# Optimization experiments

Measured on AMD Instinct MI355X. Metric: run time of the kernel, lower is better.

Reference implementation:

```python
import jax, jax.numpy as jnp
import numpy as np

EPS = 1e-13

def masked_softmax(x, mask):
    # Non-memory-efficient path of the original: softmax(x*mask), re-mask, renormalize.
    p = jax.nn.softmax(x * mask, axis=-1) * mask
    return p / (jnp.sum(p, axis=-1, keepdims=True) + EPS)

def setup_inputs() -> dict:
    key = jax.random.key(0)
    ka, kb, kma, kmb = jax.random.split(key, 4)
    B, La, Lb, D = 32, 1024, 1024, 256
    a = jax.random.normal(ka, (B, La, D), dtype=jnp.float32)
    b = jax.random.normal(kb, (B, Lb, D), dtype=jnp.float32)
    mask_a = jax.random.randint(kma, (B, La, 1), 0, 2, dtype=jnp.int32)
    mask_b = jax.random.randint(kmb, (B, Lb, 1), 0, 2, dtype=jnp.int32)
    return {"a": a, "b": b, "mask_a": mask_a, "mask_b": mask_b}

def reference(a, b, mask_a, mask_b):
    # a: [B, La, D], b: [B, Lb, D], mask_a: [B, La, 1], mask_b: [B, Lb, 1]
    ma = mask_a.astype(a.dtype)  # [B, La, 1]
    mb = mask_b.astype(b.dtype)  # [B, Lb, 1]
    attn = jnp.einsum('bid,bjd->bij', a, b)            # [B, La, Lb]
    amask = ma * jnp.swapaxes(mb, 1, 2)                 # outer product mask [B, La, Lb]
    weight_for_a = masked_softmax(attn, amask)          # softmax over Lb
    attended_a = jnp.einsum('bij,bjd->bid', weight_for_a, b)  # [B, La, D]
    attn_t = jnp.swapaxes(attn, 1, 2)                   # [B, Lb, La]
    amask_t = jnp.swapaxes(amask, 1, 2)
    weight_for_b = masked_softmax(attn_t, amask_t)      # softmax over La
    attended_b = jnp.einsum('bji,bid->bjd', weight_for_b, a)  # [B, Lb, D]
    return (attended_a, attended_b)
```

## Files before the change

### kernel.cpp

```cpp
#include <hip/hip_runtime.h>
#include <math.h>
#include <stdint.h>


#define NB    32
#define SEQ   1024
#define DIM   256
#define BM    128
#define BN    64
#define SHIFT 60.0f
#define PS    1048

typedef unsigned int uint;
typedef unsigned short ushort;
typedef __attribute__((ext_vector_type(8)))  short short8;
typedef __attribute__((ext_vector_type(16))) float f32x16;

#define HL_BATCH  (64 * 1024 * 8)
#define HL_TENSOR ((size_t)NB * HL_BATCH)
#define T_BATCH   (128 * 256 * 8)
#define T_TENSOR  ((size_t)NB * T_BATCH)
#define WS_NEED   ((2 * HL_TENSOR + 2 * T_TENSOR) * sizeof(ushort))

__device__ __forceinline__ ushort bf16_rn(float x) {
    union { float f; uint u; } v; v.f = x;
    uint r = v.u + 0x7fffu + ((v.u >> 16) & 1u);
    return (ushort)(r >> 16);
}
__device__ __forceinline__ float bf16_to_f(ushort h) {
    union { uint u; float f; } v; v.u = ((uint)h) << 16;
    return v.f;
}
__device__ __forceinline__ void gl_lds16(const ushort* g, ushort* l) {
    __builtin_amdgcn_global_load_lds(
        (const __attribute__((address_space(1))) void*)g,
        (__attribute__((address_space(3))) void*)l, 16, 0, 0);
}

#define TSTR 264
__global__ __launch_bounds__(256)
void prepass(const float* __restrict__ A, const float* __restrict__ Bt,
             ushort* __restrict__ aHL, ushort* __restrict__ bHL,
             ushort* __restrict__ aT,  ushort* __restrict__ bT)
{
    const int tensor = blockIdx.z;
    const float* src = tensor ? Bt : A;
    ushort* hl = tensor ? bHL : aHL;
    ushort* tp = tensor ? bT  : aT;
    const int batch = blockIdx.y;
    const int tid   = threadIdx.x;

    __shared__ float tile[8 * TSTR];

    ushort* hlb = hl + (size_t)batch * HL_BATCH;

    for (int it = 0; it < 8; ++it) {
        const int soct = blockIdx.x * 8 + it;
        const int s0   = soct * 8;
        if (it) __syncthreads();

        {
            const int oct = tid >> 3, srow = tid & 7;
            const float* rp = src + ((size_t)batch * SEQ + s0 + srow) * DIM + oct * 8;
            float4 x0 = *(const float4*)rp;
            float4 x1 = *(const float4*)(rp + 4);
            float xs[8] = {x0.x, x0.y, x0.z, x0.w, x1.x, x1.y, x1.z, x1.w};
            short8 hv, lv;
            #pragma unroll
            for (int j = 0; j < 8; ++j) {
                ushort h = bf16_rn(xs[j]);
                hv[j] = (short)h;
                lv[j] = (short)bf16_rn(xs[j] - bf16_to_f(h));
            }
            *(short8*)(hlb + (size_t)oct * 8192 + (size_t)(s0 + srow) * 8)        = hv;
            *(short8*)(hlb + (size_t)(oct + 32) * 8192 + (size_t)(s0 + srow) * 8) = lv;
        }

        const float* sb = src + ((size_t)batch * SEQ + s0) * DIM;
        #pragma unroll
        for (int i = 0; i < 2; ++i) {
            int idx = tid + i * 256;
            int r = idx >> 6, c = idx & 63;
            float4 v = *((const float4*)(sb + (size_t)r * DIM) + c);
            *(float4*)&tile[r * TSTR + c * 4] = v;
        }
        __syncthreads();
        {
            ushort* tpb = tp + (size_t)batch * T_BATCH + (size_t)soct * 2048;
            int d = tid;
            short8 hv;
            #pragma unroll
            for (int j = 0; j < 8; ++j)
                hv[j] = (short)bf16_rn(tile[j * TSTR + d]);
            *(short8*)(tpb + (size_t)d * 8) = hv;
        }
    }
}

__global__ __launch_bounds__(512, 2)
void attend3(const ushort* __restrict__ aHL, const ushort* __restrict__ bHL,
             const ushort* __restrict__ aT,  const ushort* __restrict__ bT,
             const int*    __restrict__ ma,  const int*    __restrict__ mb,
             float*        __restrict__ out)
{
    __shared__ __align__(16) ushort Ks2[64 * 512];
    __shared__ __align__(16) ushort Vt2[8 * 2048];
    __shared__ __align__(16) ushort Ph[8 * PS];
    __shared__ float msk[SEQ];
    __shared__ float lpart[2][BM];
    __shared__ float invs[BM];

    const int bx   = blockIdx.x;
    const int xcd  = bx & 7;
    const int slot = bx >> 3;
    const int rb   = slot & 7;
    const int pg   = slot >> 3;
    const int pair = xcd + 8 * pg;
    const int batch = pair >> 1;
    const int dir   = pair & 1;
    const int row0  = rb * BM;

    const ushort* hlX = dir ? bHL : aHL;
    const ushort* hlY = dir ? aHL : bHL;
    const ushort* tY  = dir ? aT  : bT;
    const int*    mx  = dir ? mb  : ma;
    const int*    my  = dir ? ma  : mb;
    float* o = out + (size_t)dir * NB * SEQ * DIM;

    const int tid  = threadIdx.x;
    const int lane = tid & 63;
    const int wave = tid >> 6;
    const int l31  = lane & 31;
    const int lh   = lane >> 5;
    const int rw   = wave >> 1;
    const int cw   = wave & 1;

    const ushort* hlXb = hlX + (size_t)batch * HL_BATCH;
    const ushort* hlYb = hlY + (size_t)batch * HL_BATCH;
    const ushort* tYb  = tY  + (size_t)batch * T_BATCH;

    const ushort* ksrc = hlYb + (size_t)(wave * 8) * 8192 + (size_t)lane * 8;
    ushort*       kdst = Ks2 + wave * 8 * 512 + lane * 8;
    const ushort* vsrc = tYb + (size_t)wave * 2048 + (size_t)lane * 8;
    ushort*       vdst = Vt2 + wave * 2048 + lane * 8;

    #pragma unroll
    for (int i = 0; i < 8; ++i) gl_lds16(ksrc + (size_t)i * 8192, kdst + i * 512);
    #pragma unroll
    for (int i = 0; i < 4; ++i) gl_lds16(vsrc + i * 512, vdst + i * 512);

    for (int i = tid; i < SEQ; i += 512) msk[i] = (float)my[batch * SEQ + i];

    const int qrow = row0 + rw * 32 + l31;
    short8 qhi[16], qlo[16];
    {
        const ushort* qb = hlXb + (size_t)lh * 8192 + (size_t)qrow * 8;
        #pragma unroll
        for (int kk = 0; kk < 16; ++kk) {
            qhi[kk] = *(const short8*)(qb + (size_t)(2 * kk) * 8192);
            qlo[kk] = *(const short8*)(qb + (size_t)(2 * kk + 32) * 8192);
        }
    }

    f32x16 oacc[4];
    #pragma unroll
    for (int t = 0; t < 4; ++t)
        #pragma unroll
        for (int r = 0; r < 16; ++r) oacc[t][r] = 0.f;
    float lsum[16];
    #pragma unroll
    for (int r = 0; r < 16; ++r) lsum[r] = 0.f;

    __syncthreads();

    for (int nt = 0; nt < SEQ / BN; ++nt) {
        const int key0 = nt * BN;
        const float mkv = msk[key0 + cw * 32 + l31];

        f32x16 a1, a2;
        #pragma unroll
        for (int r = 0; r < 16; ++r) { a1[r] = 0.f; a2[r] = 0.f; }
        const int kcol = (cw * 32 + l31) * 8;
        #pragma unroll
        for (int kk = 0; kk < 16; ++kk) {
            short8 bhi = *(const short8*)&Ks2[(2 * kk + lh) * 512 + kcol];
            a1 = __builtin_amdgcn_mfma_f32_32x32x16_bf16(qhi[kk], bhi, a1, 0, 0, 0);
            a2 = __builtin_amdgcn_mfma_f32_32x32x16_bf16(qlo[kk], bhi, a2, 0, 0, 0);
        }
        #pragma unroll
        for (int kk = 0; kk < 16; ++kk) {
            short8 blo = *(const short8*)&Ks2[(2 * kk + lh + 32) * 512 + kcol];
            a2 = __builtin_amdgcn_mfma_f32_32x32x16_bf16(qhi[kk], blo, a2, 0, 0, 0);
        }

        const int key  = cw * 32 + l31;
        const int koct = key >> 3, kj = key & 7;
        #pragma unroll
        for (int r = 0; r < 16; ++r) {
            float s = a1[r] + a2[r];
            float p = __expf(s - SHIFT) * mkv;
            lsum[r] += p;
            int qr = rw * 32 + (r & 3) + ((r >> 2) << 3) + (lh << 2);
            Ph[koct * PS + qr * 8 + kj] = bf16_rn(p);
        }
        __syncthreads();

        if (nt + 1 < SEQ / BN) {
            const ushort* ks = ksrc + (size_t)(key0 + BN) * 8;
            #pragma unroll
            for (int i = 0; i < 8; ++i) gl_lds16(ks + (size_t)i * 8192, kdst + i * 512);
        }

        const int prow = (rw * 32 + l31) * 8;
        #pragma unroll
        for (int kb = 0; kb < 4; ++kb) {
            short8 pa = *(const short8*)&Ph[(2 * kb + lh) * PS + prow];
            #pragma unroll
            for (int t = 0; t < 4; ++t) {
                int dim = cw * 128 + t * 32 + l31;
                short8 vf = *(const short8*)&Vt2[(2 * kb + lh) * 2048 + dim * 8];
                oacc[t] = __builtin_amdgcn_mfma_f32_32x32x16_bf16(pa, vf, oacc[t], 0, 0, 0);
            }
        }
        __syncthreads();

        if (nt + 1 < SEQ / BN) {
            const ushort* vs = vsrc + ((size_t)(key0 + BN) >> 3) * 2048;
            #pragma unroll
            for (int i = 0; i < 4; ++i) gl_lds16(vs + i * 512, vdst + i * 512);
        }
    }

    #pragma unroll
    for (int r = 0; r < 16; ++r) {
        float v = lsum[r];
        v += __shfl_xor(v, 1, 64);
        v += __shfl_xor(v, 2, 64);
        v += __shfl_xor(v, 4, 64);
        v += __shfl_xor(v, 8, 64);
        v += __shfl_xor(v, 16, 64);
        if (l31 == 0) {
            int row = rw * 32 + (r & 3) + ((r >> 2) << 3) + (lh << 2);
            lpart[cw][row] = v;
        }
    }
    __syncthreads();
    if (tid < BM) {
        float l = lpart[0][tid] + lpart[1][tid];
        int valid = mx[batch * SEQ + row0 + tid];
        invs[tid] = (valid != 0 && l > 0.f) ? 1.f / l : 0.f;
    }
    __syncthreads();

    float* ob = o + ((size_t)batch * SEQ + row0) * DIM;
    #pragma unroll
    for (int r = 0; r < 16; ++r) {
        int rloc = rw * 32 + (r & 3) + ((r >> 2) << 3) + (lh << 2);
        float inv = invs[rloc];
        #pragma unroll
        for (int t = 0; t < 4; ++t) {
            int d = cw * 128 + t * 32 + l31;
            ob[(size_t)rloc * DIM + d] = oacc[t][r] * inv;
        }
    }
}

#define F_KS_STR 520
#define F_P_STR  136
#define F_BM 64
#define F_BN 64
__global__ __launch_bounds__(256, 1)
void attend_mfma(const float* __restrict__ X, const float* __restrict__ Y,
                 const int* __restrict__ mx, const int* __restrict__ my,
                 float* __restrict__ out)
{
    __shared__ ushort Ks[F_BN * F_KS_STR];
    __shared__ ushort Ps[F_BM * F_P_STR];
    __shared__ float  mk[F_BN];
    __shared__ float  lpart[2][F_BM];
    __shared__ float  invs[F_BM];

    const int tid = threadIdx.x, lane = tid & 63, wave = tid >> 6;
    const int l31 = lane & 31, lh = lane >> 5;
    const int rw = wave >> 1, cw = wave & 1;
    const int batch = blockIdx.y, row0 = blockIdx.x * F_BM;
    const float* Xb = X + (size_t)batch * SEQ * DIM;
    const float* Yb = Y + (size_t)batch * SEQ * DIM;

    float4 kreg[16]; int mreg = 0;
    #pragma unroll
    for (int i = 0; i < 16; ++i) {
        int idx = tid + (i << 8); int r = idx >> 6, c4 = idx & 63;
        kreg[i] = *((const float4*)(Yb + (size_t)r * DIM) + c4);
    }
    if (tid < F_BN) mreg = my[batch * SEQ + tid];

    short8 qhi[16], qlo[16];
    {
        const float* qrow = Xb + (size_t)(row0 + rw * 32 + l31) * DIM + lh * 8;
        #pragma unroll
        for (int kk = 0; kk < 16; ++kk) {
            const float* p = qrow + kk * 16;
            float4 x0 = *(const float4*)p; float4 x1 = *(const float4*)(p + 4);
            float xs[8] = {x0.x, x0.y, x0.z, x0.w, x1.x, x1.y, x1.z, x1.w};
            #pragma unroll
            for (int j = 0; j < 8; ++j) {
                ushort h = bf16_rn(xs[j]);
                qhi[kk][j] = (short)h;
                qlo[kk][j] = (short)bf16_rn(xs[j] - bf16_to_f(h));
            }
        }
    }
    f32x16 oacc[4];
    #pragma unroll
    for (int t = 0; t < 4; ++t)
        #pragma unroll
        for (int r = 0; r < 16; ++r) oacc[t][r] = 0.f;
    float lsum[16];
    #pragma unroll
    for (int r = 0; r < 16; ++r) lsum[r] = 0.f;

    for (int nt = 0; nt < SEQ / F_BN; ++nt) {
        if (nt) __syncthreads();
        #pragma unroll
        for (int i = 0; i < 16; ++i) {
            int idx = tid + (i << 8); int r = idx >> 6, c4 = idx & 63;
            float f[4] = {kreg[i].x, kreg[i].y, kreg[i].z, kreg[i].w};
            ushort hh[4], ll[4];
            #pragma unroll
            for (int q = 0; q < 4; ++q) { hh[q] = bf16_rn(f[q]); ll[q] = bf16_rn(f[q] - bf16_to_f(hh[q])); }
            ushort4 hv; hv.x=hh[0];hv.y=hh[1];hv.z=hh[2];hv.w=hh[3];
            ushort4 lv; lv.x=ll[0];lv.y=ll[1];lv.z=ll[2];lv.w=ll[3];
            *(ushort4*)&Ks[r * F_KS_STR + c4 * 4] = hv;
            *(ushort4*)&Ks[r * F_KS_STR + 256 + c4 * 4] = lv;
        }
        if (tid < F_BN) mk[tid] = (float)mreg;
        __syncthreads();
        if (nt + 1 < SEQ / F_BN) {
            const float* Ybn = Yb + (size_t)(nt + 1) * F_BN * DIM;
            #pragma unroll
            for (int i = 0; i < 16; ++i) {
                int idx = tid + (i << 8); int r = idx >> 6, c4 = idx & 63;
                kreg[i] = *((const float4*)(Ybn + (size_t)r * DIM) + c4);
            }
            if (tid < F_BN) mreg = my[batch * SEQ + (nt + 1) * F_BN + tid];
        }
        f32x16 a1, a2, a3;
        #pragma unroll
        for (int r = 0; r < 16; ++r) { a1[r]=0.f; a2[r]=0.f; a3[r]=0.f; }
        const int krow = (cw * 32 + l31) * F_KS_STR;
        #pragma unroll
        for (int kk = 0; kk < 16; ++kk) {
            int col = kk * 16 + lh * 8;
            short8 bhi = *(const short8*)&Ks[krow + col];
            short8 blo = *(const short8*)&Ks[krow + 256 + col];
            a1 = __builtin_amdgcn_mfma_f32_32x32x16_bf16(qhi[kk], bhi, a1, 0, 0, 0);
            a2 = __builtin_amdgcn_mfma_f32_32x32x16_bf16(qlo[kk], bhi, a2, 0, 0, 0);
            a3 = __builtin_amdgcn_mfma_f32_32x32x16_bf16(qhi[kk], blo, a3, 0, 0, 0);
        }
        const float mkv = mk[cw * 32 + l31];
        #pragma unroll
        for (int r = 0; r < 16; ++r) {
            float s = a1[r] + a2[r] + a3[r];
            float p = __expf(s - SHIFT) * mkv;
            lsum[r] += p;
            ushort ph = bf16_rn(p);
            ushort pl = bf16_rn(p - bf16_to_f(ph));
            int prow = rw * 32 + (r & 3) + ((r >> 2) << 3) + (lh << 2);
            int pcol = cw * 32 + l31;
            Ps[prow * F_P_STR + pcol] = ph;
            Ps[prow * F_P_STR + 64 + pcol] = pl;
        }
        __syncthreads();
        const int prow = (rw * 32 + l31) * F_P_STR;
        #pragma unroll
        for (int kb = 0; kb < 4; ++kb) {
            int pcol = kb * 16 + lh * 8;
            short8 pa_hi = *(const short8*)&Ps[prow + pcol];
            short8 pa_lo = *(const short8*)&Ps[prow + 64 + pcol];
            #pragma unroll
            for (int t = 0; t < 4; ++t) {
                int d0 = cw * 128 + t * 32 + l31;
                short8 vf;
                #pragma unroll
                for (int j = 0; j < 8; ++j) vf[j] = (short)Ks[(pcol + j) * F_KS_STR + d0];
                oacc[t] = __builtin_amdgcn_mfma_f32_32x32x16_bf16(pa_hi, vf, oacc[t], 0, 0, 0);
                oacc[t] = __builtin_amdgcn_mfma_f32_32x32x16_bf16(pa_lo, vf, oacc[t], 0, 0, 0);
            }
        }
    }
    #pragma unroll
    for (int r = 0; r < 16; ++r) {
        float v = lsum[r];
        v += __shfl_xor(v, 1, 64); v += __shfl_xor(v, 2, 64); v += __shfl_xor(v, 4, 64);
        v += __shfl_xor(v, 8, 64); v += __shfl_xor(v, 16, 64);
        if (l31 == 0) {
            int row = rw * 32 + (r & 3) + ((r >> 2) << 3) + (lh << 2);
            lpart[cw][row] = v;
        }
    }
    __syncthreads();
    if (tid < F_BM) {
        float l = lpart[0][tid] + lpart[1][tid];
        int valid = mx[batch * SEQ + row0 + tid];
        invs[tid] = (valid != 0 && l > 0.f) ? 1.f / l : 0.f;
    }
    __syncthreads();
    float* ob = out + ((size_t)batch * SEQ + row0) * DIM;
    #pragma unroll
    for (int r = 0; r < 16; ++r) {
        int rloc = rw * 32 + (r & 3) + ((r >> 2) << 3) + (lh << 2);
        float inv = invs[rloc];
        #pragma unroll
        for (int t = 0; t < 4; ++t) {
            int d = cw * 128 + t * 32 + l31;
            ob[(size_t)rloc * DIM + d] = oacc[t][r] * inv;
        }
    }
}

extern "C" void kernel_launch(void* const* d_in, const int* in_sizes, int n_in,
                              void* d_out, int out_size, void* d_ws, size_t ws_size,
                              hipStream_t stream) {
    const float* a  = (const float*)d_in[0];
    const float* b  = (const float*)d_in[1];
    const int*   ma = (const int*)d_in[2];
    const int*   mb = (const int*)d_in[3];
    float* out = (float*)d_out;

    if (ws_size >= WS_NEED) {
        ushort* wsu = (ushort*)d_ws;
        ushort* aHL = wsu;
        ushort* bHL = wsu + HL_TENSOR;
        ushort* aT  = wsu + 2 * HL_TENSOR;
        ushort* bT  = wsu + 2 * HL_TENSOR + T_TENSOR;

        prepass<<<dim3(SEQ / 64, NB, 2), 256, 0, stream>>>(a, b, aHL, bHL, aT, bT);
        attend3<<<dim3(512, 1, 1), 512, 0, stream>>>(aHL, bHL, aT, bT, ma, mb, out);
    } else {
        float* out_a = out;
        float* out_b = out + (size_t)NB * SEQ * DIM;
        dim3 grid(SEQ / F_BM, NB), block(256);
        attend_mfma<<<grid, block, 0, stream>>>(a, b, ma, mb, out_a);
        attend_mfma<<<grid, block, 0, stream>>>(b, a, mb, ma, out_b);
    }
}
```

Baseline: 329.3 us.

## Use fp8 MFMA for split-precision low-part correction and stream V from global

Replaces the bf16 hi/lo split correction terms with fp8 residuals scaled by 256, so the two lo*hi cross terms run as fp8 MFMAs whose operands are loaded directly from global memory. V tiles and the key mask are also read from global instead of being staged in LDS, and the softmax-sum scratch now reuses the P buffer. Together these shrink LDS use enough to raise the launch-bounds occupancy target to 4 blocks. The prepass is restructured to stage one 64-row tile per block and emit the bf16 hi, packed fp8 residuals and transposed V. Risks are reduced accuracy from fp8 residuals and more uncached global traffic inside the inner loop.

```diff
diff --git a/kernel.cpp b/kernel.cpp
--- a/kernel.cpp
+++ b/kernel.cpp
@@ -9,18 +9,22 @@
 #define BM    128
 #define BN    64
 #define SHIFT 60.0f
-#define PS    1048
+#define PS    1032
 
 typedef unsigned int uint;
 typedef unsigned short ushort;
+typedef unsigned char uchar;
 typedef __attribute__((ext_vector_type(8)))  short short8;
 typedef __attribute__((ext_vector_type(16))) float f32x16;
-
-#define HL_BATCH  (64 * 1024 * 8)
-#define HL_TENSOR ((size_t)NB * HL_BATCH)
-#define T_BATCH   (128 * 256 * 8)
-#define T_TENSOR  ((size_t)NB * T_BATCH)
-#define WS_NEED   ((2 * HL_TENSOR + 2 * T_TENSOR) * sizeof(ushort))
+typedef __attribute__((ext_vector_type(2)))  long long ll2;
+
+#define HI_BATCH   (32 * 1024 * 8)
+#define HI_TENSOR  ((size_t)NB * HI_BATCH)
+#define F8_BATCH   (32 * 1024 * 16)
+#define F8_TENSOR  ((size_t)NB * F8_BATCH)
+#define T_BATCH    (128 * 256 * 8)
+#define T_TENSOR   ((size_t)NB * T_BATCH)
+#define WS_NEED    (2 * (HI_TENSOR * 2 + F8_TENSOR + T_TENSOR * 2))
 
 __device__ __forceinline__ ushort bf16_rn(float x) {
     union { float f; uint u; } v; v.f = x;
@@ -37,78 +41,90 @@
         (__attribute__((address_space(3))) void*)l, 16, 0, 0);
 }
 
-#define TSTR 264
+#define TSTR 260
 __global__ __launch_bounds__(256)
 void prepass(const float* __restrict__ A, const float* __restrict__ Bt,
-             ushort* __restrict__ aHL, ushort* __restrict__ bHL,
+             ushort* __restrict__ aHI, ushort* __restrict__ bHI,
+             uchar*  __restrict__ a8,  uchar*  __restrict__ b8,
              ushort* __restrict__ aT,  ushort* __restrict__ bT)
 {
     const int tensor = blockIdx.z;
     const float* src = tensor ? Bt : A;
-    ushort* hl = tensor ? bHL : aHL;
+    ushort* hi = tensor ? bHI : aHI;
+    uchar*  f8 = tensor ? b8  : a8;
     ushort* tp = tensor ? bT  : aT;
     const int batch = blockIdx.y;
+    const int s0    = blockIdx.x * 64;
     const int tid   = threadIdx.x;
 
-    __shared__ float tile[8 * TSTR];
-
-    ushort* hlb = hl + (size_t)batch * HL_BATCH;
-
-    for (int it = 0; it < 8; ++it) {
-        const int soct = blockIdx.x * 8 + it;
-        const int s0   = soct * 8;
-        if (it) __syncthreads();
-
-        {
-            const int oct = tid >> 3, srow = tid & 7;
-            const float* rp = src + ((size_t)batch * SEQ + s0 + srow) * DIM + oct * 8;
-            float4 x0 = *(const float4*)rp;
-            float4 x1 = *(const float4*)(rp + 4);
-            float xs[8] = {x0.x, x0.y, x0.z, x0.w, x1.x, x1.y, x1.z, x1.w};
-            short8 hv, lv;
+    __shared__ float tile[64 * TSTR];
+
+    const float* sb = src + ((size_t)batch * SEQ + s0) * DIM;
+    #pragma unroll
+    for (int i = 0; i < 16; ++i) {
+        int idx = tid + i * 256;
+        int r = idx >> 6, c = idx & 63;
+        float4 v = *((const float4*)(sb + (size_t)r * DIM) + c);
+        *(float4*)&tile[r * TSTR + c * 4] = v;
+    }
+    __syncthreads();
+
+    {
+        const int w = tid >> 6, lane = tid & 63;
+        ushort* hib = hi + (size_t)batch * HI_BATCH;
+        uchar*  f8b = f8 + (size_t)batch * F8_BATCH;
+        #pragma unroll
+        for (int dd = 0; dd < 8; ++dd) {
+            const int d = w * 8 + dd;
+            float4 x0 = *(const float4*)&tile[lane * TSTR + d * 8];
+            float4 x1 = *(const float4*)&tile[lane * TSTR + d * 8 + 4];
+            float f[8] = {x0.x, x0.y, x0.z, x0.w, x1.x, x1.y, x1.z, x1.w};
+            short8 hv;
+            float hf[8], lf[8];
             #pragma unroll
             for (int j = 0; j < 8; ++j) {
-                ushort h = bf16_rn(xs[j]);
+                ushort h = bf16_rn(f[j]);
                 hv[j] = (short)h;
-                lv[j] = (short)bf16_rn(xs[j] - bf16_to_f(h));
+                hf[j] = bf16_to_f(h);
+                lf[j] = (f[j] - hf[j]) * 256.0f;
             }
-            *(short8*)(hlb + (size_t)oct * 8192 + (size_t)(s0 + srow) * 8)        = hv;
-            *(short8*)(hlb + (size_t)(oct + 32) * 8192 + (size_t)(s0 + srow) * 8) = lv;
-        }
-
-        const float* sb = src + ((size_t)batch * SEQ + s0) * DIM;
-        #pragma unroll
-        for (int i = 0; i < 2; ++i) {
-            int idx = tid + i * 256;
-            int r = idx >> 6, c = idx & 63;
-            float4 v = *((const float4*)(sb + (size_t)r * DIM) + c);
-            *(float4*)&tile[r * TSTR + c * 4] = v;
-        }
-        __syncthreads();
-        {
-            ushort* tpb = tp + (size_t)batch * T_BATCH + (size_t)soct * 2048;
-            int d = tid;
+            uint h0 = __builtin_amdgcn_cvt_pk_fp8_f32(hf[0], hf[1], 0u, false);
+            h0      = __builtin_amdgcn_cvt_pk_fp8_f32(hf[2], hf[3], h0, true);
+            uint h1 = __builtin_amdgcn_cvt_pk_fp8_f32(hf[4], hf[5], 0u, false);
+            h1      = __builtin_amdgcn_cvt_pk_fp8_f32(hf[6], hf[7], h1, true);
+            uint l0 = __builtin_amdgcn_cvt_pk_fp8_f32(lf[0], lf[1], 0u, false);
+            l0      = __builtin_amdgcn_cvt_pk_fp8_f32(lf[2], lf[3], l0, true);
+            uint l1 = __builtin_amdgcn_cvt_pk_fp8_f32(lf[4], lf[5], 0u, false);
+            l1      = __builtin_amdgcn_cvt_pk_fp8_f32(lf[6], lf[7], l1, true);
+            *(short8*)(hib + (size_t)d * 8192 + (size_t)(s0 + lane) * 8) = hv;
+            uint4 pk; pk.x = h0; pk.y = h1; pk.z = l0; pk.w = l1;
+            *(uint4*)(f8b + (size_t)d * 16384 + (size_t)(s0 + lane) * 16) = pk;
+        }
+    }
+
+    {
+        ushort* tpb = tp + (size_t)batch * T_BATCH;
+        const int d = tid;
+        #pragma unroll
+        for (int so = 0; so < 8; ++so) {
             short8 hv;
             #pragma unroll
             for (int j = 0; j < 8; ++j)
-                hv[j] = (short)bf16_rn(tile[j * TSTR + d]);
-            *(short8*)(tpb + (size_t)d * 8) = hv;
-        }
-    }
-}
-
-__global__ __launch_bounds__(512, 2)
-void attend3(const ushort* __restrict__ aHL, const ushort* __restrict__ bHL,
+                hv[j] = (short)bf16_rn(tile[(so * 8 + j) * TSTR + d]);
+            *(short8*)(tpb + (size_t)(blockIdx.x * 8 + so) * 2048 + (size_t)d * 8) = hv;
+        }
+    }
+}
+
+__global__ __launch_bounds__(512, 4)
+void attend4(const ushort* __restrict__ aHI, const ushort* __restrict__ bHI,
+             const uchar*  __restrict__ a8,  const uchar*  __restrict__ b8,
              const ushort* __restrict__ aT,  const ushort* __restrict__ bT,
              const int*    __restrict__ ma,  const int*    __restrict__ mb,
              float*        __restrict__ out)
 {
-    __shared__ __align__(16) ushort Ks2[64 * 512];
-    __shared__ __align__(16) ushort Vt2[8 * 2048];
+    __shared__ __align__(16) ushort KhiS[32 * 512];
     __shared__ __align__(16) ushort Ph[8 * PS];
-    __shared__ float msk[SEQ];
-    __shared__ float lpart[2][BM];
-    __shared__ float invs[BM];
 
     const int bx   = blockIdx.x;
     const int xcd  = bx & 7;
@@ -120,9 +136,11 @@
     const int dir   = pair & 1;
     const int row0  = rb * BM;
 
-    const ushort* hlX = dir ? bHL : aHL;
-    const ushort* hlY = dir ? aHL : bHL;
-    const ushort* tY  = dir ? aT  : bT;
+    const ushort* xhi = dir ? bHI : aHI;
+    const uchar*  x8  = dir ? b8  : a8;
+    const ushort* yhi = dir ? aHI : bHI;
+    const uchar*  y8  = dir ? a8  : b8;
+    const ushort* yt  = dir ? aT  : bT;
     const int*    mx  = dir ? mb  : ma;
     const int*    my  = dir ? ma  : mb;
     float* o = out + (size_t)dir * NB * SEQ * DIM;
@@ -135,32 +153,26 @@
     const int rw   = wave >> 1;
     const int cw   = wave & 1;
 
-    const ushort* hlXb = hlX + (size_t)batch * HL_BATCH;
-    const ushort* hlYb = hlY + (size_t)batch * HL_BATCH;
-    const ushort* tYb  = tY  + (size_t)batch * T_BATCH;
-
-    const ushort* ksrc = hlYb + (size_t)(wave * 8) * 8192 + (size_t)lane * 8;
-    ushort*       kdst = Ks2 + wave * 8 * 512 + lane * 8;
-    const ushort* vsrc = tYb + (size_t)wave * 2048 + (size_t)lane * 8;
-    ushort*       vdst = Vt2 + wave * 2048 + lane * 8;
-
-    #pragma unroll
-    for (int i = 0; i < 8; ++i) gl_lds16(ksrc + (size_t)i * 8192, kdst + i * 512);
-    #pragma unroll
-    for (int i = 0; i < 4; ++i) gl_lds16(vsrc + i * 512, vdst + i * 512);
-
-    for (int i = tid; i < SEQ; i += 512) msk[i] = (float)my[batch * SEQ + i];
+    const ushort* xhib = xhi + (size_t)batch * HI_BATCH;
+    const uchar*  x8b  = x8  + (size_t)batch * F8_BATCH;
+    const ushort* yhib = yhi + (size_t)batch * HI_BATCH;
+    const uchar*  y8b  = y8  + (size_t)batch * F8_BATCH;
+    const ushort* ytb  = yt  + (size_t)batch * T_BATCH;
+
+    const ushort* ksrc = yhib + (size_t)(wave * 4) * 8192 + (size_t)lane * 8;
+    ushort*       kdst = KhiS + wave * 4 * 512 + lane * 8;
+    #pragma unroll
+    for (int i = 0; i < 4; ++i) gl_lds16(ksrc + (size_t)i * 8192, kdst + i * 512);
 
     const int qrow = row0 + rw * 32 + l31;
-    short8 qhi[16], qlo[16];
+    short8 qhi[16];
     {
-        const ushort* qb = hlXb + (size_t)lh * 8192 + (size_t)qrow * 8;
-        #pragma unroll
-        for (int kk = 0; kk < 16; ++kk) {
+        const ushort* qb = xhib + (size_t)lh * 8192 + (size_t)qrow * 8;
+        #pragma unroll
+        for (int kk = 0; kk < 16; ++kk)
             qhi[kk] = *(const short8*)(qb + (size_t)(2 * kk) * 8192);
-            qlo[kk] = *(const short8*)(qb + (size_t)(2 * kk + 32) * 8192);
-        }
-    }
+    }
+    const uchar* q8base = x8b + (size_t)lh * 16384 + (size_t)qrow * 16;
 
     f32x16 oacc[4];
     #pragma unroll
@@ -173,31 +185,30 @@
 
     __syncthreads();
 
+    const int key  = cw * 32 + l31;
+    const int koct = key >> 3, kj = key & 7;
+
     for (int nt = 0; nt < SEQ / BN; ++nt) {
         const int key0 = nt * BN;
-        const float mkv = msk[key0 + cw * 32 + l31];
+        const float mkv = (float)my[batch * SEQ + key0 + key];
 
         f32x16 a1, a2;
         #pragma unroll
         for (int r = 0; r < 16; ++r) { a1[r] = 0.f; a2[r] = 0.f; }
-        const int kcol = (cw * 32 + l31) * 8;
+        const uchar* k8base = y8b + (size_t)lh * 16384 + (size_t)(key0 + key) * 16;
         #pragma unroll
         for (int kk = 0; kk < 16; ++kk) {
-            short8 bhi = *(const short8*)&Ks2[(2 * kk + lh) * 512 + kcol];
+            short8 bhi = *(const short8*)&KhiS[(2 * kk + lh) * 512 + key * 8];
+            ll2 k8 = *(const ll2*)(k8base + (size_t)(2 * kk) * 16384);
+            ll2 q8 = *(const ll2*)(q8base + (size_t)(2 * kk) * 16384);
             a1 = __builtin_amdgcn_mfma_f32_32x32x16_bf16(qhi[kk], bhi, a1, 0, 0, 0);
-            a2 = __builtin_amdgcn_mfma_f32_32x32x16_bf16(qlo[kk], bhi, a2, 0, 0, 0);
-        }
-        #pragma unroll
-        for (int kk = 0; kk < 16; ++kk) {
-            short8 blo = *(const short8*)&Ks2[(2 * kk + lh + 32) * 512 + kcol];
-            a2 = __builtin_amdgcn_mfma_f32_32x32x16_bf16(qhi[kk], blo, a2, 0, 0, 0);
-        }
-
-        const int key  = cw * 32 + l31;
-        const int koct = key >> 3, kj = key & 7;
+            a2 = __builtin_amdgcn_mfma_f32_32x32x16_fp8_fp8(q8.y, k8.x, a2, 0, 0, 0);
+            a2 = __builtin_amdgcn_mfma_f32_32x32x16_fp8_fp8(q8.x, k8.y, a2, 0, 0, 0);
+        }
+
         #pragma unroll
         for (int r = 0; r < 16; ++r) {
-            float s = a1[r] + a2[r];
+            float s = a1[r] + a2[r] * 0.00390625f;
             float p = __expf(s - SHIFT) * mkv;
             lsum[r] += p;
             int qr = rw * 32 + (r & 3) + ((r >> 2) << 3) + (lh << 2);
@@ -208,29 +219,26 @@
         if (nt + 1 < SEQ / BN) {
             const ushort* ks = ksrc + (size_t)(key0 + BN) * 8;
             #pragma unroll
-            for (int i = 0; i < 8; ++i) gl_lds16(ks + (size_t)i * 8192, kdst + i * 512);
+            for (int i = 0; i < 4; ++i) gl_lds16(ks + (size_t)i * 8192, kdst + i * 512);
         }
 
         const int prow = (rw * 32 + l31) * 8;
         #pragma unroll
         for (int kb = 0; kb < 4; ++kb) {
             short8 pa = *(const short8*)&Ph[(2 * kb + lh) * PS + prow];
+            const ushort* vb = ytb + (size_t)(nt * 8 + 2 * kb + lh) * 2048;
             #pragma unroll
             for (int t = 0; t < 4; ++t) {
                 int dim = cw * 128 + t * 32 + l31;
-                short8 vf = *(const short8*)&Vt2[(2 * kb + lh) * 2048 + dim * 8];
+                short8 vf = *(const short8*)(vb + (size_t)dim * 8);
                 oacc[t] = __builtin_amdgcn_mfma_f32_32x32x16_bf16(pa, vf, oacc[t], 0, 0, 0);
             }
         }
         __syncthreads();
-
-        if (nt + 1 < SEQ / BN) {
-            const ushort* vs = vsrc + ((size_t)(key0 + BN) >> 3) * 2048;
-            #pragma unroll
-            for (int i = 0; i < 4; ++i) gl_lds16(vs + i * 512, vdst + i * 512);
-        }
-    }
-
+    }
+
+    float* lp = (float*)Ph;
+    float* iv = lp + 2 * BM;
     #pragma unroll
     for (int r = 0; r < 16; ++r) {
         float v = lsum[r];
@@ -241,14 +249,14 @@
         v += __shfl_xor(v, 16, 64);
         if (l31 == 0) {
             int row = rw * 32 + (r & 3) + ((r >> 2) << 3) + (lh << 2);
-            lpart[cw][row] = v;
+            lp[cw * BM + row] = v;
         }
     }
     __syncthreads();
     if (tid < BM) {
-        float l = lpart[0][tid] + lpart[1][tid];
+        float l = lp[tid] + lp[BM + tid];
         int valid = mx[batch * SEQ + row0 + tid];
-        invs[tid] = (valid != 0 && l > 0.f) ? 1.f / l : 0.f;
+        iv[tid] = (valid != 0 && l > 0.f) ? 1.f / l : 0.f;
     }
     __syncthreads();
 
@@ -256,7 +264,7 @@
     #pragma unroll
     for (int r = 0; r < 16; ++r) {
         int rloc = rw * 32 + (r & 3) + ((r >> 2) << 3) + (lh << 2);
-        float inv = invs[rloc];
+        float inv = iv[rloc];
         #pragma unroll
         for (int t = 0; t < 4; ++t) {
             int d = cw * 128 + t * 32 + l31;
@@ -429,14 +437,16 @@
     float* out = (float*)d_out;
 
     if (ws_size >= WS_NEED) {
-        ushort* wsu = (ushort*)d_ws;
-        ushort* aHL = wsu;
-        ushort* bHL = wsu + HL_TENSOR;
-        ushort* aT  = wsu + 2 * HL_TENSOR;
-        ushort* bT  = wsu + 2 * HL_TENSOR + T_TENSOR;
-
-        prepass<<<dim3(SEQ / 64, NB, 2), 256, 0, stream>>>(a, b, aHL, bHL, aT, bT);
-        attend3<<<dim3(512, 1, 1), 512, 0, stream>>>(aHL, bHL, aT, bT, ma, mb, out);
+        char* w = (char*)d_ws;
+        ushort* aHI = (ushort*)w;
+        ushort* bHI = (ushort*)(w + 16 * 1024 * 1024);
+        uchar*  a8  = (uchar*) (w + 32 * 1024 * 1024);
+        uchar*  b8  = (uchar*) (w + 48 * 1024 * 1024);
+        ushort* aT  = (ushort*)(w + 64 * 1024 * 1024);
+        ushort* bT  = (ushort*)(w + 80 * 1024 * 1024);
+
+        prepass<<<dim3(SEQ / 64, NB, 2), 256, 0, stream>>>(a, b, aHI, bHI, a8, b8, aT, bT);
+        attend4<<<dim3(512, 1, 1), 512, 0, stream>>>(aHI, bHI, a8, b8, aT, bT, ma, mb, out);
     } else {
         float* out_a = out;
         float* out_b = out + (size_t)NB * SEQ * DIM;
```

Measured after the change: 759.6 us. 131% more time.

## Restructure attention kernel to 4 waves with register-resident P and split hi/lo buffers

Applied to the files above, without the earlier changes.

Replaces the 8-wave attend3 kernel with a 4-wave attend6. Each wave now owns 32 query rows across all 256 output dims and all 64 keys per tile. The score MFMAs are transposed so that the probability fragment is rearranged in registers with a cross-half shuffle, which removes the LDS round-trip for P and one barrier per tile. K hi/lo tiles are double-buffered in LDS through async global-to-LDS loads, while V fragments are read directly from global memory. The prepass also processes 32 rows per block and writes separate hi/lo arrays. The trade-offs are higher register pressure (8 output accumulators), one block per SM, and uncached global reads of V inside the loop.

```diff
diff --git a/kernel.cpp b/kernel.cpp
--- a/kernel.cpp
+++ b/kernel.cpp
@@ -9,18 +9,17 @@
 #define BM    128
 #define BN    64
 #define SHIFT 60.0f
-#define PS    1048
 
 typedef unsigned int uint;
 typedef unsigned short ushort;
 typedef __attribute__((ext_vector_type(8)))  short short8;
 typedef __attribute__((ext_vector_type(16))) float f32x16;
 
-#define HL_BATCH  (64 * 1024 * 8)
-#define HL_TENSOR ((size_t)NB * HL_BATCH)
+#define HI_BATCH  (32 * 1024 * 8)
+#define HI_TENSOR ((size_t)NB * HI_BATCH)
 #define T_BATCH   (128 * 256 * 8)
 #define T_TENSOR  ((size_t)NB * T_BATCH)
-#define WS_NEED   ((2 * HL_TENSOR + 2 * T_TENSOR) * sizeof(ushort))
+#define WS_NEED   (6 * HI_TENSOR * sizeof(ushort))
 
 __device__ __forceinline__ ushort bf16_rn(float x) {
     union { float f; uint u; } v; v.f = x;
@@ -37,78 +36,82 @@
         (__attribute__((address_space(3))) void*)l, 16, 0, 0);
 }
 
-#define TSTR 264
+#define TSTR 260
 __global__ __launch_bounds__(256)
 void prepass(const float* __restrict__ A, const float* __restrict__ Bt,
-             ushort* __restrict__ aHL, ushort* __restrict__ bHL,
-             ushort* __restrict__ aT,  ushort* __restrict__ bT)
+             ushort* __restrict__ aHI, ushort* __restrict__ aLO, ushort* __restrict__ aT,
+             ushort* __restrict__ bHI, ushort* __restrict__ bLO, ushort* __restrict__ bT)
 {
     const int tensor = blockIdx.z;
     const float* src = tensor ? Bt : A;
-    ushort* hl = tensor ? bHL : aHL;
+    ushort* hi = tensor ? bHI : aHI;
+    ushort* lo = tensor ? bLO : aLO;
     ushort* tp = tensor ? bT  : aT;
     const int batch = blockIdx.y;
+    const int s0    = blockIdx.x * 32;
     const int tid   = threadIdx.x;
 
-    __shared__ float tile[8 * TSTR];
-
-    ushort* hlb = hl + (size_t)batch * HL_BATCH;
-
-    for (int it = 0; it < 8; ++it) {
-        const int soct = blockIdx.x * 8 + it;
-        const int s0   = soct * 8;
-        if (it) __syncthreads();
-
-        {
-            const int oct = tid >> 3, srow = tid & 7;
+    __shared__ float tile[32 * TSTR];
+
+    const float* sb = src + ((size_t)batch * SEQ + s0) * DIM;
+    #pragma unroll
+    for (int i = 0; i < 8; ++i) {
+        int idx = tid + i * 256;
+        int r = idx >> 6, c = idx & 63;
+        float4 v = *((const float4*)(sb + (size_t)r * DIM) + c);
+        *(float4*)&tile[r * TSTR + c * 4] = v;
+    }
+
+    {
+        ushort* hib = hi + (size_t)batch * HI_BATCH;
+        ushort* lob = lo + (size_t)batch * HI_BATCH;
+        const int oct = tid >> 3;
+        #pragma unroll
+        for (int rr = 0; rr < 4; ++rr) {
+            const int srow = (tid & 7) + rr * 8;
             const float* rp = src + ((size_t)batch * SEQ + s0 + srow) * DIM + oct * 8;
             float4 x0 = *(const float4*)rp;
             float4 x1 = *(const float4*)(rp + 4);
-            float xs[8] = {x0.x, x0.y, x0.z, x0.w, x1.x, x1.y, x1.z, x1.w};
+            float f[8] = {x0.x, x0.y, x0.z, x0.w, x1.x, x1.y, x1.z, x1.w};
             short8 hv, lv;
             #pragma unroll
             for (int j = 0; j < 8; ++j) {
-                ushort h = bf16_rn(xs[j]);
-                hv[j] = (short)h;
-                lv[j] = (short)bf16_rn(xs[j] - bf16_to_f(h));
-            }
-            *(short8*)(hlb + (size_t)oct * 8192 + (size_t)(s0 + srow) * 8)        = hv;
-            *(short8*)(hlb + (size_t)(oct + 32) * 8192 + (size_t)(s0 + srow) * 8) = lv;
-        }
-
-        const float* sb = src + ((size_t)batch * SEQ + s0) * DIM;
-        #pragma unroll
-        for (int i = 0; i < 2; ++i) {
-            int idx = tid + i * 256;
-            int r = idx >> 6, c = idx & 63;
-            float4 v = *((const float4*)(sb + (size_t)r * DIM) + c);
-            *(float4*)&tile[r * TSTR + c * 4] = v;
-        }
-        __syncthreads();
-        {
-            ushort* tpb = tp + (size_t)batch * T_BATCH + (size_t)soct * 2048;
-            int d = tid;
+                ushort hh = bf16_rn(f[j]);
+                hv[j] = (short)hh;
+                lv[j] = (short)bf16_rn(f[j] - bf16_to_f(hh));
+            }
+            *(short8*)(hib + (size_t)oct * 8192 + (size_t)(s0 + srow) * 8) = hv;
+            *(short8*)(lob + (size_t)oct * 8192 + (size_t)(s0 + srow) * 8) = lv;
+        }
+    }
+    __syncthreads();
+
+    {
+        ushort* tpb = tp + (size_t)batch * T_BATCH;
+        const int d = tid;
+        #pragma unroll
+        for (int so = 0; so < 4; ++so) {
             short8 hv;
             #pragma unroll
             for (int j = 0; j < 8; ++j)
-                hv[j] = (short)bf16_rn(tile[j * TSTR + d]);
-            *(short8*)(tpb + (size_t)d * 8) = hv;
-        }
-    }
-}
-
-__global__ __launch_bounds__(512, 2)
-void attend3(const ushort* __restrict__ aHL, const ushort* __restrict__ bHL,
-             const ushort* __restrict__ aT,  const ushort* __restrict__ bT,
+                hv[j] = (short)bf16_rn(tile[(so * 8 + j) * TSTR + d]);
+            *(short8*)(tpb + (size_t)(blockIdx.x * 4 + so) * 2048 + (size_t)d * 8) = hv;
+        }
+    }
+}
+
+__global__ __launch_bounds__(256, 1)
+void attend6(const ushort* __restrict__ aHI, const ushort* __restrict__ aLO,
+             const ushort* __restrict__ aT,
+             const ushort* __restrict__ bHI, const ushort* __restrict__ bLO,
+             const ushort* __restrict__ bT,
              const int*    __restrict__ ma,  const int*    __restrict__ mb,
              float*        __restrict__ out)
 {
-    __shared__ __align__(16) ushort Ks2[64 * 512];
-    __shared__ __align__(16) ushort Vt2[8 * 2048];
-    __shared__ __align__(16) ushort Ph[8 * PS];
+    __shared__ __align__(16) ushort KhiS[2 * 32 * 512];
+    __shared__ __align__(16) ushort KloS[2 * 32 * 512];
     __shared__ float msk[SEQ];
-    __shared__ float lpart[2][BM];
-    __shared__ float invs[BM];
+    __shared__ float ivs[BM];
 
     const int bx   = blockIdx.x;
     const int xcd  = bx & 7;
@@ -120,9 +123,11 @@
     const int dir   = pair & 1;
     const int row0  = rb * BM;
 
-    const ushort* hlX = dir ? bHL : aHL;
-    const ushort* hlY = dir ? aHL : bHL;
-    const ushort* tY  = dir ? aT  : bT;
+    const ushort* xHI = dir ? bHI : aHI;
+    const ushort* xLO = dir ? bLO : aLO;
+    const ushort* yHI = dir ? aHI : bHI;
+    const ushort* yLO = dir ? aLO : bLO;
+    const ushort* yT  = dir ? aT  : bT;
     const int*    mx  = dir ? mb  : ma;
     const int*    my  = dir ? ma  : mb;
     float* o = out + (size_t)dir * NB * SEQ * DIM;
@@ -131,137 +136,136 @@
     const int lane = tid & 63;
     const int wave = tid >> 6;
     const int l31  = lane & 31;
-    const int lh   = lane >> 5;
-    const int rw   = wave >> 1;
-    const int cw   = wave & 1;
-
-    const ushort* hlXb = hlX + (size_t)batch * HL_BATCH;
-    const ushort* hlYb = hlY + (size_t)batch * HL_BATCH;
-    const ushort* tYb  = tY  + (size_t)batch * T_BATCH;
-
-    const ushort* ksrc = hlYb + (size_t)(wave * 8) * 8192 + (size_t)lane * 8;
-    ushort*       kdst = Ks2 + wave * 8 * 512 + lane * 8;
-    const ushort* vsrc = tYb + (size_t)wave * 2048 + (size_t)lane * 8;
-    ushort*       vdst = Vt2 + wave * 2048 + lane * 8;
-
-    #pragma unroll
-    for (int i = 0; i < 8; ++i) gl_lds16(ksrc + (size_t)i * 8192, kdst + i * 512);
-    #pragma unroll
-    for (int i = 0; i < 4; ++i) gl_lds16(vsrc + i * 512, vdst + i * 512);
-
-    for (int i = tid; i < SEQ; i += 512) msk[i] = (float)my[batch * SEQ + i];
-
-    const int qrow = row0 + rw * 32 + l31;
+    const int h    = lane >> 5;
+
+    const ushort* xHIb = xHI + (size_t)batch * HI_BATCH;
+    const ushort* xLOb = xLO + (size_t)batch * HI_BATCH;
+    const ushort* yHIb = yHI + (size_t)batch * HI_BATCH;
+    const ushort* yLOb = yLO + (size_t)batch * HI_BATCH;
+    const ushort* yTb  = yT  + (size_t)batch * T_BATCH;
+
+    #pragma unroll
+    for (int i = 0; i < 8; ++i) {
+        const int doct = wave * 8 + i;
+        gl_lds16(yHIb + (size_t)doct * 8192 + (size_t)lane * 8, KhiS + doct * 512 + lane * 8);
+        gl_lds16(yLOb + (size_t)doct * 8192 + (size_t)lane * 8, KloS + doct * 512 + lane * 8);
+    }
+    for (int i = tid; i < SEQ; i += 256) msk[i] = (float)my[batch * SEQ + i];
+
+    const int qrow = row0 + wave * 32 + l31;
     short8 qhi[16], qlo[16];
     {
-        const ushort* qb = hlXb + (size_t)lh * 8192 + (size_t)qrow * 8;
+        const ushort* qh = xHIb + (size_t)h * 8192 + (size_t)qrow * 8;
+        const ushort* ql = xLOb + (size_t)h * 8192 + (size_t)qrow * 8;
         #pragma unroll
         for (int kk = 0; kk < 16; ++kk) {
-            qhi[kk] = *(const short8*)(qb + (size_t)(2 * kk) * 8192);
-            qlo[kk] = *(const short8*)(qb + (size_t)(2 * kk + 32) * 8192);
-        }
-    }
-
-    f32x16 oacc[4];
-    #pragma unroll
-    for (int t = 0; t < 4; ++t)
+            qhi[kk] = *(const short8*)(qh + (size_t)(2 * kk) * 8192);
+            qlo[kk] = *(const short8*)(ql + (size_t)(2 * kk) * 8192);
+        }
+    }
+
+    f32x16 oacc[8];
+    #pragma unroll
+    for (int t = 0; t < 8; ++t)
         #pragma unroll
         for (int r = 0; r < 16; ++r) oacc[t][r] = 0.f;
-    float lsum[16];
-    #pragma unroll
-    for (int r = 0; r < 16; ++r) lsum[r] = 0.f;
+    float lsum = 0.f;
 
     __syncthreads();
 
     for (int nt = 0; nt < SEQ / BN; ++nt) {
+        const int cur  = nt & 1;
         const int key0 = nt * BN;
-        const float mkv = msk[key0 + cw * 32 + l31];
-
-        f32x16 a1, a2;
-        #pragma unroll
-        for (int r = 0; r < 16; ++r) { a1[r] = 0.f; a2[r] = 0.f; }
-        const int kcol = (cw * 32 + l31) * 8;
+        const ushort* kh = KhiS + cur * (32 * 512);
+        const ushort* kl = KloS + cur * (32 * 512);
+
+        if (nt + 1 < SEQ / BN) {
+            ushort* nh = KhiS + (cur ^ 1) * (32 * 512);
+            ushort* nl = KloS + (cur ^ 1) * (32 * 512);
+            #pragma unroll
+            for (int i = 0; i < 8; ++i) {
+                const int doct = wave * 8 + i;
+                gl_lds16(yHIb + (size_t)doct * 8192 + (size_t)(key0 + BN + lane) * 8,
+                         nh + doct * 512 + lane * 8);
+                gl_lds16(yLOb + (size_t)doct * 8192 + (size_t)(key0 + BN + lane) * 8,
+                         nl + doct * 512 + lane * 8);
+            }
+        }
+
+        f32x16 c0h, c0c, c1h, c1c;
+        #pragma unroll
+        for (int r = 0; r < 16; ++r) { c0h[r] = 0.f; c0c[r] = 0.f; c1h[r] = 0.f; c1c[r] = 0.f; }
         #pragma unroll
         for (int kk = 0; kk < 16; ++kk) {
-            short8 bhi = *(const short8*)&Ks2[(2 * kk + lh) * 512 + kcol];
-            a1 = __builtin_amdgcn_mfma_f32_32x32x16_bf16(qhi[kk], bhi, a1, 0, 0, 0);
-            a2 = __builtin_amdgcn_mfma_f32_32x32x16_bf16(qlo[kk], bhi, a2, 0, 0, 0);
-        }
-        #pragma unroll
-        for (int kk = 0; kk < 16; ++kk) {
-            short8 blo = *(const short8*)&Ks2[(2 * kk + lh + 32) * 512 + kcol];
-            a2 = __builtin_amdgcn_mfma_f32_32x32x16_bf16(qhi[kk], blo, a2, 0, 0, 0);
-        }
-
-        const int key  = cw * 32 + l31;
-        const int koct = key >> 3, kj = key & 7;
+            const int off = (2 * kk + h) * 512;
+            short8 k0h = *(const short8*)&kh[off + l31 * 8];
+            short8 k1h = *(const short8*)&kh[off + (32 + l31) * 8];
+            short8 k0l = *(const short8*)&kl[off + l31 * 8];
+            short8 k1l = *(const short8*)&kl[off + (32 + l31) * 8];
+            c0h = __builtin_amdgcn_mfma_f32_32x32x16_bf16(k0h, qhi[kk], c0h, 0, 0, 0);
+            c1h = __builtin_amdgcn_mfma_f32_32x32x16_bf16(k1h, qhi[kk], c1h, 0, 0, 0);
+            c0c = __builtin_amdgcn_mfma_f32_32x32x16_bf16(k0l, qhi[kk], c0c, 0, 0, 0);
+            c0c = __builtin_amdgcn_mfma_f32_32x32x16_bf16(k0h, qlo[kk], c0c, 0, 0, 0);
+            c1c = __builtin_amdgcn_mfma_f32_32x32x16_bf16(k1l, qhi[kk], c1c, 0, 0, 0);
+            c1c = __builtin_amdgcn_mfma_f32_32x32x16_bf16(k1h, qlo[kk], c1c, 0, 0, 0);
+        }
+
+        float pe[2][16];
         #pragma unroll
         for (int r = 0; r < 16; ++r) {
-            float s = a1[r] + a2[r];
-            float p = __expf(s - SHIFT) * mkv;
-            lsum[r] += p;
-            int qr = rw * 32 + (r & 3) + ((r >> 2) << 3) + (lh << 2);
-            Ph[koct * PS + qr * 8 + kj] = bf16_rn(p);
-        }
+            const int kloc = (r & 3) + 8 * (r >> 2) + 4 * h;
+            float m0 = msk[key0 + kloc];
+            float m1 = msk[key0 + 32 + kloc];
+            float p0 = __expf(c0h[r] + c0c[r] - SHIFT) * m0;
+            float p1 = __expf(c1h[r] + c1c[r] - SHIFT) * m1;
+            lsum += p0 + p1;
+            pe[0][r] = p0;
+            pe[1][r] = p1;
+        }
+
+        short8 pf[4];
+        #pragma unroll
+        for (int kb = 0; kb < 4; ++kb) {
+            #pragma unroll
+            for (int j = 0; j < 4; ++j) {
+                float x = pe[kb >> 1][8 * (kb & 1) + j];
+                float y = pe[kb >> 1][8 * (kb & 1) + 4 + j];
+                float send = h ? x : y;
+                float recv = __shfl_xor(send, 32, 64);
+                float aj  = h ? recv : x;
+                float aj4 = h ? y : recv;
+                pf[kb][j]     = (short)bf16_rn(aj);
+                pf[kb][j + 4] = (short)bf16_rn(aj4);
+            }
+        }
+
+        #pragma unroll
+        for (int kb = 0; kb < 4; ++kb) {
+            const ushort* vb = yTb + (size_t)(nt * 8 + 2 * kb + h) * 2048;
+            #pragma unroll
+            for (int t = 0; t < 8; ++t) {
+                short8 vf = *(const short8*)(vb + (size_t)(t * 32 + l31) * 8);
+                oacc[t] = __builtin_amdgcn_mfma_f32_32x32x16_bf16(pf[kb], vf, oacc[t], 0, 0, 0);
+            }
+        }
+
         __syncthreads();
-
-        if (nt + 1 < SEQ / BN) {
-            const ushort* ks = ksrc + (size_t)(key0 + BN) * 8;
-            #pragma unroll
-            for (int i = 0; i < 8; ++i) gl_lds16(ks + (size_t)i * 8192, kdst + i * 512);
-        }
-
-        const int prow = (rw * 32 + l31) * 8;
-        #pragma unroll
-        for (int kb = 0; kb < 4; ++kb) {
-            short8 pa = *(const short8*)&Ph[(2 * kb + lh) * PS + prow];
-            #pragma unroll
-            for (int t = 0; t < 4; ++t) {
-                int dim = cw * 128 + t * 32 + l31;
-                short8 vf = *(const short8*)&Vt2[(2 * kb + lh) * 2048 + dim * 8];
-                oacc[t] = __builtin_amdgcn_mfma_f32_32x32x16_bf16(pa, vf, oacc[t], 0, 0, 0);
-            }
-        }
-        __syncthreads();
-
-        if (nt + 1 < SEQ / BN) {
-            const ushort* vs = vsrc + ((size_t)(key0 + BN) >> 3) * 2048;
-            #pragma unroll
-            for (int i = 0; i < 4; ++i) gl_lds16(vs + i * 512, vdst + i * 512);
-        }
-    }
-
+    }
+
+    float ltot = lsum + __shfl_xor(lsum, 32, 64);
+    if (lane < 32) {
+        int row = wave * 32 + lane;
+        int valid = mx[batch * SEQ + row0 + row];
+        ivs[row] = (valid != 0 && ltot > 0.f) ? 1.f / ltot : 0.f;
+    }
+    float* ob = o + ((size_t)batch * SEQ + row0 + wave * 32) * DIM;
     #pragma unroll
     for (int r = 0; r < 16; ++r) {
-        float v = lsum[r];
-        v += __shfl_xor(v, 1, 64);
-        v += __shfl_xor(v, 2, 64);
-        v += __shfl_xor(v, 4, 64);
-        v += __shfl_xor(v, 8, 64);
-        v += __shfl_xor(v, 16, 64);
-        if (l31 == 0) {
-            int row = rw * 32 + (r & 3) + ((r >> 2) << 3) + (lh << 2);
-            lpart[cw][row] = v;
-        }
-    }
-    __syncthreads();
-    if (tid < BM) {
-        float l = lpart[0][tid] + lpart[1][tid];
-        int valid = mx[batch * SEQ + row0 + tid];
-        invs[tid] = (valid != 0 && l > 0.f) ? 1.f / l : 0.f;
-    }
-    __syncthreads();
-
-    float* ob = o + ((size_t)batch * SEQ + row0) * DIM;
-    #pragma unroll
-    for (int r = 0; r < 16; ++r) {
-        int rloc = rw * 32 + (r & 3) + ((r >> 2) << 3) + (lh << 2);
-        float inv = invs[rloc];
-        #pragma unroll
-        for (int t = 0; t < 4; ++t) {
-            int d = cw * 128 + t * 32 + l31;
-            ob[(size_t)rloc * DIM + d] = oacc[t][r] * inv;
-        }
+        const int rl = (r & 3) + 8 * (r >> 2) + 4 * h;
+        float inv = ivs[wave * 32 + rl];
+        #pragma unroll
+        for (int t = 0; t < 8; ++t)
+            ob[(size_t)rl * DIM + t * 32 + l31] = oacc[t][r] * inv;
     }
 }
 
@@ -305,9 +309,9 @@
             float xs[8] = {x0.x, x0.y, x0.z, x0.w, x1.x, x1.y, x1.z, x1.w};
             #pragma unroll
             for (int j = 0; j < 8; ++j) {
-                ushort h = bf16_rn(xs[j]);
-                qhi[kk][j] = (short)h;
-                qlo[kk][j] = (short)bf16_rn(xs[j] - bf16_to_f(h));
+                ushort hh = bf16_rn(xs[j]);
+                qhi[kk][j] = (short)hh;
+                qlo[kk][j] = (short)bf16_rn(xs[j] - bf16_to_f(hh));
             }
         }
     }
@@ -429,14 +433,16 @@
     float* out = (float*)d_out;
 
     if (ws_size >= WS_NEED) {
-        ushort* wsu = (ushort*)d_ws;
-        ushort* aHL = wsu;
-        ushort* bHL = wsu + HL_TENSOR;
-        ushort* aT  = wsu + 2 * HL_TENSOR;
-        ushort* bT  = wsu + 2 * HL_TENSOR + T_TENSOR;
-
-        prepass<<<dim3(SEQ / 64, NB, 2), 256, 0, stream>>>(a, b, aHL, bHL, aT, bT);
-        attend3<<<dim3(512, 1, 1), 512, 0, stream>>>(aHL, bHL, aT, bT, ma, mb, out);
+        char* w = (char*)d_ws;
+        ushort* aHI = (ushort*)(w + 0 * 16 * 1024 * 1024);
+        ushort* aLO = (ushort*)(w + 1 * 16 * 1024 * 1024);
+        ushort* aT  = (ushort*)(w + 2 * 16 * 1024 * 1024);
+        ushort* bHI = (ushort*)(w + 3 * 16 * 1024 * 1024);
+        ushort* bLO = (ushort*)(w + 4 * 16 * 1024 * 1024);
+        ushort* bT  = (ushort*)(w + 5 * 16 * 1024 * 1024);
+
+        prepass<<<dim3(SEQ / 32, NB, 2), 256, 0, stream>>>(a, b, aHI, aLO, aT, bHI, bLO, bT);
+        attend6<<<dim3(512, 1, 1), 256, 0, stream>>>(aHI, aLO, aT, bHI, bLO, bT, ma, mb, out);
     } else {
         float* out_a = out;
         float* out_b = out + (size_t)NB * SEQ * DIM;
```

Measured after the change: 508.9 us. 1.55x slower.
